# Optimization experiments

Hardware: AMD Instinct MI355X
Metric: run time of the kernel (lower is better)

The kernel has to match this reference:

```python
import jax, jax.numpy as jnp
import numpy as np

N, H, G = 8192, 256, 256


def setup_inputs() -> dict:
    key = jax.random.key(0)
    ks = jax.random.split(key, 12)
    s = 1.0 / np.sqrt(H)
    inp = {
        "x": jax.random.normal(ks[0], (N, H), dtype=jnp.float32),
        "batch": jnp.sort(jax.random.randint(ks[1], (N,), 0, G)),
        "num_graphs": G,
        "aw": jax.random.uniform(ks[2], (H, H), jnp.float32, -s, s),
        "ab": jax.random.uniform(ks[3], (H,), jnp.float32, -s, s),
        "p1w": jax.random.uniform(ks[4], (H, H), jnp.float32, -s, s),
        "p1b": jax.random.uniform(ks[5], (H,), jnp.float32, -s, s),
        "p2w": jax.random.uniform(ks[6], (H, H), jnp.float32, -s, s),
        "p2b": jax.random.uniform(ks[7], (H,), jnp.float32, -s, s),
        "r1w": jax.random.uniform(ks[8], (H, H), jnp.float32, -s, s),
        "r1b": jax.random.uniform(ks[9], (H,), jnp.float32, -s, s),
        "r2w": jax.random.uniform(ks[10], (H, H), jnp.float32, -s, s),
        "r2b": jax.random.uniform(ks[11], (H,), jnp.float32, -s, s),
    }
    return inp


def reference(x, batch, num_graphs, aw, ab, p1w, p1b, p2w, p2b, r1w, r1b, r2w, r2b):
    # phi: two Linear+ReLU layers
    h = jax.nn.relu(jax.nn.relu(x @ p1w + p1b) @ p2w + p2b)          # [N, H]
    s = h @ aw + ab                                                  # attention scores [N, H]
    dot = s @ s.T                                                    # [N, N]
    mask = (batch[:, None] == batch[None, :]).astype(dot.dtype)      # block-diagonal [N, N]
    # hand-rolled masked softmax exactly as in the torch module
    max_vals = jnp.max(dot * mask, axis=1, keepdims=True)            # [N, 1]
    masked_dot = (dot - max_vals) * mask
    e = jnp.exp(masked_dot)
    attn = e / jnp.sum(e * mask, axis=1, keepdims=True) * mask       # [N, N]
    x_weighted = attn @ h                                            # [N, H]
    x_agg = jax.ops.segment_sum(x_weighted, batch, num_segments=num_graphs)  # [G, H]
    # rho: two Linear+ReLU layers
    out = jax.nn.relu(jax.nn.relu(x_agg @ r1w + r1b) @ r2w + r2b)    # [G, H]
    return out
```

## Files before the change

### kernel.cpp

```cpp
#include <hip/hip_runtime.h>
#include <hip/hip_bf16.h>
#include <stdint.h>

#define NN 8192
#define HH 256
#define GG 256

typedef __bf16 bf16x8 __attribute__((ext_vector_type(8)));
typedef float f32x4 __attribute__((ext_vector_type(4)));
typedef unsigned short u16v8 __attribute__((ext_vector_type(8)));

__device__ __forceinline__ ushort f2bf(float f) {
  union { float f; uint32_t u; } v; v.f = f;
  uint32_t u = v.u;
  u += 0x7fffu + ((u >> 16) & 1u);
  return (ushort)(u >> 16);
}
__device__ __forceinline__ float bf2f(ushort h) {
  union { uint32_t u; float f; } v; v.u = ((uint32_t)h) << 16;
  return v.f;
}

__global__ __launch_bounds__(512) void k_prep(const float* __restrict__ p1w,
                                              const float* __restrict__ p2w,
                                              const float* __restrict__ aw,
                                              const float* __restrict__ r1w,
                                              const float* __restrict__ r2w,
                                              ushort* __restrict__ wT1,
                                              ushort* __restrict__ wT2,
                                              ushort* __restrict__ wTa,
                                              ushort* __restrict__ rK1,
                                              ushort* __restrict__ rK2) {
  int b = blockIdx.x, t = threadIdx.x;
  if (b < 48) {
    int mat = b >> 4, tile = b & 15;
    int tr = (tile >> 2) * 64, tc = (tile & 3) * 64;
    const float* w = mat == 0 ? p1w : mat == 1 ? p2w : aw;
    ushort* o = mat == 0 ? wT1 : mat == 1 ? wT2 : wTa;
    __shared__ float tileb[64][65];
    int rr = t >> 3, cg = (t & 7) * 8;
    const float* src = w + (size_t)(tr + rr) * HH + tc + cg;
    float4 v0 = *(const float4*)src;
    float4 v1 = *(const float4*)(src + 4);
    float* drow = &tileb[rr][cg];
    drow[0] = v0.x; drow[1] = v0.y; drow[2] = v0.z; drow[3] = v0.w;
    drow[4] = v1.x; drow[5] = v1.y; drow[6] = v1.z; drow[7] = v1.w;
    __syncthreads();
    int rn = t >> 3, kg = (t & 7) * 8;
    u16v8 a;
#pragma unroll
    for (int j = 0; j < 8; ++j) a[j] = f2bf(tileb[kg + j][rn]);
    *(u16v8*)(o + (size_t)(tc + rn) * HH + tr + kg) = a;
  } else {
    int eb = b - 48;
    const float* src = (eb < 8) ? r1w : r2w;
    ushort* dst = (eb < 8) ? rK1 : rK2;
    int sub = eb & 7;
#pragma unroll
    for (int it = 0; it < 2; ++it) {
      int base = sub * 8192 + it * 4096 + t * 8;
      float4 v0 = *(const float4*)(src + base);
      float4 v1 = *(const float4*)(src + base + 4);
      u16v8 o;
      o[0] = f2bf(v0.x); o[1] = f2bf(v0.y); o[2] = f2bf(v0.z); o[3] = f2bf(v0.w);
      o[4] = f2bf(v1.x); o[5] = f2bf(v1.y); o[6] = f2bf(v1.z); o[7] = f2bf(v1.w);
      *(u16v8*)(dst + base) = o;
    }
  }
}

__global__ __launch_bounds__(1024, 4) void k_main(
    const float* __restrict__ x, const int* __restrict__ batch,
    const float* __restrict__ ab,
    const float* __restrict__ p1b, const float* __restrict__ p2b,
    const float* __restrict__ r1b, const float* __restrict__ r2b,
    const ushort* __restrict__ wT1, const ushort* __restrict__ wT2,
    const ushort* __restrict__ wTa,
    const ushort* __restrict__ rK1, const ushort* __restrict__ rK2,
    float* __restrict__ out) {
  __shared__ ushort actA[16384];
  __shared__ ushort actB[16384];
  __shared__ int bb[256];
  __shared__ int mm[4];
  __shared__ float colw[256];
  __shared__ float xa[256];
  __shared__ float parts[1024];
  __shared__ float pmax[128];
  __shared__ float psum[128];
  __shared__ float fct[128];

  const int g = blockIdx.x, tid = threadIdx.x;
  const int lane = tid & 63, wid = tid >> 6;
  const int l15 = lane & 15, q = lane >> 4, x7 = l15 & 7;

  if (tid < 256) bb[tid] = batch[tid * 32];
  if (tid == 0) { mm[0] = 256; mm[1] = 256; }
  __syncthreads();
  if (tid < 256) {
    int v = bb[tid];
    int pv = (tid == 0) ? -1 : bb[tid - 1];
    if (v >= g && pv < g) mm[0] = tid;
    if (v >= g + 1 && pv < g + 1) mm[1] = tid;
  }
  __syncthreads();
  {
    int which = -1, v = 0;
    if (tid < 32) { which = 2; v = g; }
    else if (tid >= 64 && tid < 96) { which = 3; v = g + 1; }
    if (which >= 0) {
      int B = mm[which - 2];
      int u = tid & 31;
      if (B == 0) { if (u == 0) mm[which] = 0; }
      else {
        int i = (B - 1) * 32 + 1 + u;
        if (i <= 8191 && batch[i] >= v && batch[i - 1] < v) mm[which] = i;
        if (B == 256 && u == 0 && batch[8191] < v) mm[which] = 8192;
      }
    }
  }
  __syncthreads();
  const int r0 = mm[2];
  int n = mm[3] - r0;
  if (n > 64) n = 64;
  const int R = ((n + 15) >> 4) * 16;

  for (int ch = tid; ch < R * 32; ch += 1024) {
    int row = ch >> 5, c = ch & 31;
    int srow = r0 + row; if (srow > 8191) srow = 8191;
    const float* xp = x + (size_t)srow * HH + c * 8;
    float4 v0 = *(const float4*)xp;
    float4 v1 = *(const float4*)(xp + 4);
    u16v8 o;
    o[0] = f2bf(v0.x); o[1] = f2bf(v0.y); o[2] = f2bf(v0.z); o[3] = f2bf(v0.w);
    o[4] = f2bf(v1.x); o[5] = f2bf(v1.y); o[6] = f2bf(v1.z); o[7] = f2bf(v1.w);
    int dst = (ch & ~31) | (c ^ (row & 7));
    *(u16v8*)(actA + dst * 8) = o;
  }
  __syncthreads();

  const int mycol = wid * 16 + l15;
  const ushort* wrow1 = wT1 + (size_t)mycol * HH + q * 8;
  const ushort* wrow2 = wT2 + (size_t)mycol * HH + q * 8;
  const ushort* wrowa = wTa + (size_t)mycol * HH + q * 8;
  bf16x8 wA[8], wB[8];
#pragma unroll
  for (int kk = 0; kk < 8; ++kk) wA[kk] = *(const bf16x8*)(wrow1 + kk * 32);
#pragma unroll
  for (int kk = 0; kk < 8; ++kk) wB[kk] = *(const bf16x8*)(wrow2 + kk * 32);

  {
    float bv = p1b[mycol];
#pragma unroll
    for (int rt4 = 0; rt4 < 4; ++rt4) {
      if (rt4 * 16 < n) {
        f32x4 acc = {0.f, 0.f, 0.f, 0.f};
#pragma unroll
        for (int kk = 0; kk < 8; ++kk) {
          int ca = (kk * 4 + q) ^ x7;
          bf16x8 a = *(const bf16x8*)(actA + ((rt4 * 16 + l15) * 32 + ca) * 8);
          acc = __builtin_amdgcn_mfma_f32_16x16x32_bf16(a, wA[kk], acc, 0, 0, 0);
        }
#pragma unroll
        for (int i = 0; i < 4; ++i) {
          float vv = fmaxf(acc[i] + bv, 0.f);
          int r = rt4 * 16 + q * 4 + i;
          int cc = (mycol >> 3) ^ (r & 7);
          actB[(r * 32 + cc) * 8 + (mycol & 7)] = f2bf(vv);
        }
      }
    }
  }
  __syncthreads();
#pragma unroll
  for (int kk = 0; kk < 8; ++kk) wA[kk] = *(const bf16x8*)(wrowa + kk * 32);

  {
    float bv = p2b[mycol];
#pragma unroll
    for (int rt4 = 0; rt4 < 4; ++rt4) {
      if (rt4 * 16 < n) {
        f32x4 acc = {0.f, 0.f, 0.f, 0.f};
#pragma unroll
        for (int kk = 0; kk < 8; ++kk) {
          int ca = (kk * 4 + q) ^ x7;
          bf16x8 a = *(const bf16x8*)(actB + ((rt4 * 16 + l15) * 32 + ca) * 8);
          acc = __builtin_amdgcn_mfma_f32_16x16x32_bf16(a, wB[kk], acc, 0, 0, 0);
        }
#pragma unroll
        for (int i = 0; i < 4; ++i) {
          float vv = fmaxf(acc[i] + bv, 0.f);
          int r = rt4 * 16 + q * 4 + i;
          int cc = (mycol >> 3) ^ (r & 7);
          actA[(r * 32 + cc) * 8 + (mycol & 7)] = f2bf(vv);
        }
      }
    }
  }
  __syncthreads();

  {
    float bv = ab[mycol];
#pragma unroll
    for (int rt4 = 0; rt4 < 4; ++rt4) {
      if (rt4 * 16 < n) {
        f32x4 acc = {0.f, 0.f, 0.f, 0.f};
#pragma unroll
        for (int kk = 0; kk < 8; ++kk) {
          int ca = (kk * 4 + q) ^ x7;
          bf16x8 a = *(const bf16x8*)(actA + ((rt4 * 16 + l15) * 32 + ca) * 8);
          acc = __builtin_amdgcn_mfma_f32_16x16x32_bf16(a, wA[kk], acc, 0, 0, 0);
        }
#pragma unroll
        for (int i = 0; i < 4; ++i) {
          float vv = acc[i] + bv;
          int r = rt4 * 16 + q * 4 + i;
          int cc = (mycol >> 3) ^ (r & 7);
          actB[(r * 32 + cc) * 8 + (mycol & 7)] = f2bf(vv);
        }
      }
    }
  }
  __syncthreads();

  if (tid < 256) colw[tid] = 0.f;
  __syncthreads();
  const int rt = wid & 3, h2 = wid >> 2;
  const bool liveW = (wid < 8) && (rt * 16 < n);
  float e0[4], e1[4];
  int cb0 = 0, cb1 = 0;
  if (liveW) {
    const char* stc = (const char*)actB;
    cb0 = (h2 * 2 + 0) * 16; cb1 = (h2 * 2 + 1) * 16;
    f32x4 acc0 = {0.f, 0.f, 0.f, 0.f}, acc1 = acc0;
    const int arow = rt * 16 + l15;
    if (cb0 < n) {
#pragma unroll
      for (int kk = 0; kk < 8; kk++) {
        int kc = ((kk * 4 + q) ^ x7) << 4;
        bf16x8 a  = *(const bf16x8*)(stc + arow * 512 + kc);
        bf16x8 b0 = *(const bf16x8*)(stc + (cb0 + l15) * 512 + kc);
        acc0 = __builtin_amdgcn_mfma_f32_16x16x32_bf16(a, b0, acc0, 0, 0, 0);
        if (cb1 < n) {
          bf16x8 b1 = *(const bf16x8*)(stc + (cb1 + l15) * 512 + kc);
          acc1 = __builtin_amdgcn_mfma_f32_16x16x32_bf16(a, b1, acc1, 0, 0, 0);
        }
      }
    }
    float pm[4], ps[4];
#pragma unroll
    for (int i = 0; i < 4; i++) {
      float mmx = (cb0 + l15 < n) ? acc0[i] : -1e30f;
      if (cb1 + l15 < n) mmx = fmaxf(mmx, acc1[i]);
      pm[i] = mmx;
    }
#pragma unroll
    for (int off = 1; off < 16; off <<= 1)
#pragma unroll
      for (int i = 0; i < 4; i++) pm[i] = fmaxf(pm[i], __shfl_xor(pm[i], off));
#pragma unroll
    for (int i = 0; i < 4; i++) {
      e0[i] = (cb0 + l15 < n) ? __expf(acc0[i] - pm[i]) : 0.f;
      e1[i] = (cb1 + l15 < n) ? __expf(acc1[i] - pm[i]) : 0.f;
      ps[i] = e0[i] + e1[i];
    }
#pragma unroll
    for (int off = 1; off < 16; off <<= 1)
#pragma unroll
      for (int i = 0; i < 4; i++) ps[i] += __shfl_xor(ps[i], off);
    if (l15 == 0) {
#pragma unroll
      for (int i = 0; i < 4; i++) {
        int row = rt * 16 + q * 4 + i;
        pmax[h2 * 64 + row] = pm[i];
        psum[h2 * 64 + row] = ps[i];
      }
    }
  }
  __syncthreads();
  if (tid < 128) {
    int h = tid >> 6, row = tid & 63;
    float m0 = pmax[row], m1 = pmax[64 + row];
    float m = fmaxf(m0, m1);
    float S = psum[row] * __expf(m0 - m) + psum[64 + row] * __expf(m1 - m);
    fct[h * 64 + row] = (S > 0.f) ? __expf(pmax[h * 64 + row] - m) / S : 0.f;
  }
  __syncthreads();
  if (liveW) {
    float cs0 = 0.f, cs1 = 0.f;
#pragma unroll
    for (int i = 0; i < 4; i++) {
      int row = rt * 16 + q * 4 + i;
      if (row < n) {
        float f = fct[h2 * 64 + row];
        cs0 += e0[i] * f;
        cs1 += e1[i] * f;
      }
    }
    cs0 += __shfl_xor(cs0, 16); cs0 += __shfl_xor(cs0, 32);
    cs1 += __shfl_xor(cs1, 16); cs1 += __shfl_xor(cs1, 32);
    if (lane < 16) {
      if (cb0 < n) atomicAdd(&colw[cb0 + l15], cs0);
      if (cb1 < n) atomicAdd(&colw[cb1 + l15], cs1);
    }
  }
  __syncthreads();

  {
    int c = tid & 255, qr = tid >> 8;
    float agg = 0.f;
    for (int jj = qr; jj < n; jj += 4) {
      int cc = (c >> 3) ^ (jj & 7);
      agg = fmaf(colw[jj], bf2f(actA[(jj * 32 + cc) * 8 + (c & 7)]), agg);
    }
    parts[qr * 256 + c] = agg;
  }
  __syncthreads();
  if (tid < 256)
    xa[tid] = (parts[tid] + parts[256 + tid]) + (parts[512 + tid] + parts[768 + tid]);
  __syncthreads();

  {
    const int col = tid & 255, kq = tid >> 8;
    const int k0 = kq * 64;
    float a0 = 0.f, a1 = 0.f, a2 = 0.f, a3 = 0.f;
    const ushort* wp = rK1 + (size_t)k0 * HH + col;
#pragma unroll 4
    for (int k = 0; k < 64; k += 4) {
      a0 = fmaf(xa[k0 + k],     bf2f(wp[(size_t)(k)     * HH]), a0);
      a1 = fmaf(xa[k0 + k + 1], bf2f(wp[(size_t)(k + 1) * HH]), a1);
      a2 = fmaf(xa[k0 + k + 2], bf2f(wp[(size_t)(k + 2) * HH]), a2);
      a3 = fmaf(xa[k0 + k + 3], bf2f(wp[(size_t)(k + 3) * HH]), a3);
    }
    parts[kq * 256 + col] = (a0 + a1) + (a2 + a3);
    __syncthreads();
    if (tid < 256)
      colw[tid] = fmaxf(r1b[tid] + (parts[tid] + parts[256 + tid]) +
                        (parts[512 + tid] + parts[768 + tid]), 0.f);
    __syncthreads();
    a0 = a1 = a2 = a3 = 0.f;
    const ushort* wp2 = rK2 + (size_t)k0 * HH + col;
#pragma unroll 4
    for (int k = 0; k < 64; k += 4) {
      a0 = fmaf(colw[k0 + k],     bf2f(wp2[(size_t)(k)     * HH]), a0);
      a1 = fmaf(colw[k0 + k + 1], bf2f(wp2[(size_t)(k + 1) * HH]), a1);
      a2 = fmaf(colw[k0 + k + 2], bf2f(wp2[(size_t)(k + 2) * HH]), a2);
      a3 = fmaf(colw[k0 + k + 3], bf2f(wp2[(size_t)(k + 3) * HH]), a3);
    }
    parts[kq * 256 + col] = (a0 + a1) + (a2 + a3);
    __syncthreads();
    if (tid < 256)
      out[(size_t)g * HH + tid] = fmaxf(r2b[tid] + (parts[tid] + parts[256 + tid]) +
                                        (parts[512 + tid] + parts[768 + tid]), 0.f);
  }
}

extern "C" void kernel_launch(void* const* d_in, const int* in_sizes, int n_in,
                              void* d_out, int out_size, void* d_ws, size_t ws_size,
                              hipStream_t stream) {
  const float* x   = (const float*)d_in[0];
  const int* batch = (const int*)d_in[1];
  const float* aw  = (const float*)d_in[3];
  const float* ab  = (const float*)d_in[4];
  const float* p1w = (const float*)d_in[5];
  const float* p1b = (const float*)d_in[6];
  const float* p2w = (const float*)d_in[7];
  const float* p2b = (const float*)d_in[8];
  const float* r1w = (const float*)d_in[9];
  const float* r1b = (const float*)d_in[10];
  const float* r2w = (const float*)d_in[11];
  const float* r2b = (const float*)d_in[12];
  float* out = (float*)d_out;

  char* ws = (char*)d_ws;
  ushort* wT1 = (ushort*)(ws);
  ushort* wT2 = wT1 + 65536;
  ushort* wTa = wT2 + 65536;
  ushort* rK1 = wTa + 65536;
  ushort* rK2 = rK1 + 65536;

  k_prep<<<dim3(64), dim3(512), 0, stream>>>(p1w, p2w, aw, r1w, r2w,
                                             wT1, wT2, wTa, rK1, rK2);
  k_main<<<dim3(256), dim3(1024), 0, stream>>>(x, batch, ab, p1b, p2b, r1b, r2b,
                                               wT1, wT2, wTa, rK1, rK2, out);
}
```

Baseline: 34.05 us.

## Replicate converted weights, biases and batch samples into 8 workspace copies

New measurement: 34.31 us. Within noise of the previous version (+0.8%).

```diff
diff --git a/kernel.cpp b/kernel.cpp
--- a/kernel.cpp
+++ b/kernel.cpp
@@ -5,6 +5,8 @@
 #define NN 8192
 #define HH 256
 #define GG 256
+#define NCOPY 8
+#define WCOPY 327680
 
 typedef __bf16 bf16x8 __attribute__((ext_vector_type(8)));
 typedef float f32x4 __attribute__((ext_vector_type(4)));
@@ -26,17 +28,21 @@
                                               const float* __restrict__ aw,
                                               const float* __restrict__ r1w,
                                               const float* __restrict__ r2w,
-                                              ushort* __restrict__ wT1,
-                                              ushort* __restrict__ wT2,
-                                              ushort* __restrict__ wTa,
-                                              ushort* __restrict__ rK1,
-                                              ushort* __restrict__ rK2) {
+                                              const float* __restrict__ p1b,
+                                              const float* __restrict__ p2b,
+                                              const float* __restrict__ ab,
+                                              const float* __restrict__ r1b,
+                                              const float* __restrict__ r2b,
+                                              const int* __restrict__ batch,
+                                              ushort* __restrict__ wsW,
+                                              float* __restrict__ wsB,
+                                              int* __restrict__ wsI) {
   int b = blockIdx.x, t = threadIdx.x;
   if (b < 48) {
     int mat = b >> 4, tile = b & 15;
     int tr = (tile >> 2) * 64, tc = (tile & 3) * 64;
     const float* w = mat == 0 ? p1w : mat == 1 ? p2w : aw;
-    ushort* o = mat == 0 ? wT1 : mat == 1 ? wT2 : wTa;
+    size_t moff = (size_t)mat * 65536;
     __shared__ float tileb[64][65];
     int rr = t >> 3, cg = (t & 7) * 8;
     const float* src = w + (size_t)(tr + rr) * HH + tc + cg;
@@ -50,11 +56,14 @@
     u16v8 a;
 #pragma unroll
     for (int j = 0; j < 8; ++j) a[j] = f2bf(tileb[kg + j][rn]);
-    *(u16v8*)(o + (size_t)(tc + rn) * HH + tr + kg) = a;
-  } else {
+    size_t idx = moff + (size_t)(tc + rn) * HH + tr + kg;
+#pragma unroll
+    for (int c = 0; c < NCOPY; ++c)
+      *(u16v8*)(wsW + (size_t)c * WCOPY + idx) = a;
+  } else if (b < 64) {
     int eb = b - 48;
     const float* src = (eb < 8) ? r1w : r2w;
-    ushort* dst = (eb < 8) ? rK1 : rK2;
+    size_t moff = (eb < 8) ? (size_t)3 * 65536 : (size_t)4 * 65536;
     int sub = eb & 7;
 #pragma unroll
     for (int it = 0; it < 2; ++it) {
@@ -64,19 +73,29 @@
       u16v8 o;
       o[0] = f2bf(v0.x); o[1] = f2bf(v0.y); o[2] = f2bf(v0.z); o[3] = f2bf(v0.w);
       o[4] = f2bf(v1.x); o[5] = f2bf(v1.y); o[6] = f2bf(v1.z); o[7] = f2bf(v1.w);
-      *(u16v8*)(dst + base) = o;
+#pragma unroll
+      for (int c = 0; c < NCOPY; ++c)
+        *(u16v8*)(wsW + (size_t)c * WCOPY + moff + base) = o;
+    }
+  } else {
+    if (t < 256) {
+      float b0 = p1b[t], b1 = p2b[t], b2 = ab[t], b3 = r1b[t], b4 = r2b[t];
+      int s = batch[t * 32];
+#pragma unroll
+      for (int c = 0; c < NCOPY; ++c) {
+        float* bp = wsB + c * 1280;
+        bp[t] = b0; bp[256 + t] = b1; bp[512 + t] = b2;
+        bp[768 + t] = b3; bp[1024 + t] = b4;
+        wsI[c * 256 + t] = s;
+      }
     }
   }
 }
 
 __global__ __launch_bounds__(1024, 4) void k_main(
     const float* __restrict__ x, const int* __restrict__ batch,
-    const float* __restrict__ ab,
-    const float* __restrict__ p1b, const float* __restrict__ p2b,
-    const float* __restrict__ r1b, const float* __restrict__ r2b,
-    const ushort* __restrict__ wT1, const ushort* __restrict__ wT2,
-    const ushort* __restrict__ wTa,
-    const ushort* __restrict__ rK1, const ushort* __restrict__ rK2,
+    const ushort* __restrict__ wsW, const float* __restrict__ wsB,
+    const int* __restrict__ wsI,
     float* __restrict__ out) {
   __shared__ ushort actA[16384];
   __shared__ ushort actB[16384];
@@ -93,7 +112,17 @@
   const int lane = tid & 63, wid = tid >> 6;
   const int l15 = lane & 15, q = lane >> 4, x7 = l15 & 7;
 
-  if (tid < 256) bb[tid] = batch[tid * 32];
+  const ushort* wbase = wsW + (size_t)(g & (NCOPY - 1)) * WCOPY;
+  const ushort* wT1 = wbase;
+  const ushort* wT2 = wbase + 65536;
+  const ushort* wTa = wbase + 131072;
+  const ushort* rK1 = wbase + 196608;
+  const ushort* rK2 = wbase + 262144;
+  const float* bB = wsB + (g & (NCOPY - 1)) * 1280;
+  const float* p1b = bB, *p2b = bB + 256, *ab = bB + 512;
+  const float* r1b = bB + 768, *r2b = bB + 1024;
+
+  if (tid < 256) bb[tid] = wsI[(g & (NCOPY - 1)) * 256 + tid];
   if (tid == 0) { mm[0] = 256; mm[1] = 256; }
   __syncthreads();
   if (tid < 256) {
@@ -372,14 +401,12 @@
   float* out = (float*)d_out;
 
   char* ws = (char*)d_ws;
-  ushort* wT1 = (ushort*)(ws);
-  ushort* wT2 = wT1 + 65536;
-  ushort* wTa = wT2 + 65536;
-  ushort* rK1 = wTa + 65536;
-  ushort* rK2 = rK1 + 65536;
-
-  k_prep<<<dim3(64), dim3(512), 0, stream>>>(p1w, p2w, aw, r1w, r2w,
-                                             wT1, wT2, wTa, rK1, rK2);
-  k_main<<<dim3(256), dim3(1024), 0, stream>>>(x, batch, ab, p1b, p2b, r1b, r2b,
-                                               wT1, wT2, wTa, rK1, rK2, out);
+  ushort* wsW = (ushort*)(ws);
+  float*  wsB = (float*)(ws + (size_t)8 * 1024 * 1024);
+  int*    wsI = (int*)(ws + (size_t)8 * 1024 * 1024 + 64 * 1024);
+
+  k_prep<<<dim3(65), dim3(512), 0, stream>>>(p1w, p2w, aw, r1w, r2w,
+                                             p1b, p2b, ab, r1b, r2b, batch,
+                                             wsW, wsB, wsI);
+  k_main<<<dim3(256), dim3(1024), 0, stream>>>(x, batch, wsW, wsB, wsI, out);
 }
```
